# Performance work log

Hardware: AMD Instinct MI355X
Metric: run time of the kernel (lower is better)

## Reference

```python
import jax, jax.numpy as jnp
import numpy as np

N = 50000
E_RAND = 800000
IN_DIM = 256
HID = 64
HEADS = 4
OUT_DIM = 256
NEG_SLOPE = 0.01  # torch F.leaky_relu default


def _xavier(key, shape, fan_in, fan_out):
    gain = np.sqrt(2.0)  # calculate_gain('relu')
    std = gain * np.sqrt(2.0 / (fan_in + fan_out))
    return jax.random.normal(key, shape, dtype=jnp.float32) * std


def setup_inputs() -> dict:
    key = jax.random.key(0)
    k = jax.random.split(key, 8)
    h = jax.random.normal(k[0], (N, IN_DIM), dtype=jnp.float32)
    # random edges + self-loops so every node has in-degree >= 1
    src = jnp.concatenate([jax.random.randint(k[1], (E_RAND,), 0, N), jnp.arange(N)]).astype(jnp.int32)
    dst = jnp.concatenate([jax.random.randint(k[2], (E_RAND,), 0, N), jnp.arange(N)]).astype(jnp.int32)
    # layer1: HEADS independent GAT heads, hidden HID each
    W1 = _xavier(k[3], (HEADS, HID, IN_DIM), IN_DIM, HID)          # fc.weight per head
    a1 = _xavier(k[4], (HEADS, 2 * HID), 2 * HID, 1)               # attn_fc.weight per head
    # layer2: single head, in = HID*HEADS, out = OUT_DIM
    W2 = _xavier(k[5], (OUT_DIM, HID * HEADS), HID * HEADS, OUT_DIM)
    a2 = _xavier(k[6], (2 * OUT_DIM,), 2 * OUT_DIM, 1)
    return {"h": h, "W1": W1, "a1": a1, "W2": W2, "a2": a2, "src": src, "dst": dst}


def _leaky(x):
    return jnp.where(x > 0, x, NEG_SLOPE * x)


def _segment_softmax(e, dst, n):
    # e: [E, ...] logits per edge; softmax over edges sharing the same dst node
    m = jax.ops.segment_max(e, dst, num_segments=n)
    m = jnp.where(jnp.isfinite(m), m, 0.0)  # guard empty segments
    ex = jnp.exp(e - m[dst])
    s = jax.ops.segment_sum(ex, dst, num_segments=n)
    return ex / s[dst]


def reference(h, W1, a1, W2, a2, src, dst):
    n = h.shape[0]
    # ---- layer1: multi-head GAT, merge='cat' ----
    z = jnp.einsum('ni,hoi->nho', h, W1)                 # [N,H,HID]
    a_s, a_d = a1[:, :HID], a1[:, HID:]                  # split cat([src,dst]) linear
    es = jnp.einsum('nho,ho->nh', z, a_s)                # per-node src score
    ed = jnp.einsum('nho,ho->nh', z, a_d)                # per-node dst score
    e = _leaky(es[src] + ed[dst])                        # [E,H]
    alpha = _segment_softmax(e, dst, n)                  # segment softmax per dst
    m = jax.ops.segment_sum(alpha[:, :, None] * z[src], dst, num_segments=n)  # [N,H,HID]
    h1 = jax.nn.elu(m.reshape(n, HEADS * HID))
    # ---- layer2: single-head GAT ----
    z2 = h1 @ W2.T                                       # [N,OUT]
    e2 = _leaky((z2 @ a2[:OUT_DIM])[src] + (z2 @ a2[OUT_DIM:])[dst])  # [E]
    alpha2 = _segment_softmax(e2, dst, n)
    out = jax.ops.segment_sum(alpha2[:, None] * z2[src], dst, num_segments=n)  # [N,OUT]
    return out
```

## Files before the change

kernel.cpp:

```cpp
#include <hip/hip_runtime.h>
#include <hip/hip_bf16.h>
#include <math.h>

#define NEG 0.01f
#define MAXDEG 128

typedef __attribute__((ext_vector_type(4))) unsigned u32x4;
typedef __attribute__((ext_vector_type(4))) float f32x4;

__device__ __forceinline__ float wmax_all(float v){
#pragma unroll
  for (int o=32;o>0;o>>=1) v = fmaxf(v, __shfl_xor(v,o,64));
  return v;
}
__device__ __forceinline__ float wsum_all(float v){
#pragma unroll
  for (int o=32;o>0;o>>=1) v += __shfl_xor(v,o,64);
  return v;
}
__device__ __forceinline__ int wred_sum_i(int v){
#pragma unroll
  for (int o=32;o>0;o>>=1) v += __shfl_down(v,o,64);
  return v;
}
__device__ __forceinline__ float bf_lo(unsigned u){ union{unsigned i;float f;} c; c.i=u<<16; return c.f; }
__device__ __forceinline__ float bf_hi(unsigned u){ union{unsigned i;float f;} c; c.i=u&0xffff0000u; return c.f; }
__device__ __forceinline__ unsigned short f2bf(float f){
  union{float f; unsigned i;} c; c.f=f;
  unsigned r = c.i + 0x7fffu + ((c.i>>16)&1u);
  return (unsigned short)(r>>16);
}
__device__ __forceinline__ float leaky1(float x){ return x>0.f? x : NEG*x; }

__device__ __forceinline__ void mfma16(f32x4& d, u32x4 a, u32x4 b){
  asm volatile("v_mfma_f32_16x16x32_bf16 %0, %1, %2, %0" : "+v"(d) : "v"(a), "v"(b));
}

__global__ void zero_cnt_k(int* __restrict__ cnt, int n){
  int i = blockIdx.x*blockDim.x + threadIdx.x;
  if (i<n) cnt[i]=0;
}

__global__ void hist_k(const int* __restrict__ dst, int* __restrict__ cnt, int E){
  int i = blockIdx.x*blockDim.x+threadIdx.x;
  if (i<E) atomicAdd(&cnt[dst[i]], 1);
}

__global__ void scan_partial_k(const int* __restrict__ cnt, int* __restrict__ bsum, int n){
  int b = blockIdx.x, t = threadIdx.x;
  int base = b*1024 + t*4;
  int s=0;
#pragma unroll
  for (int i=0;i<4;i++){ int idx=base+i; if(idx<n) s+=cnt[idx]; }
  int ws = wred_sum_i(s);
  __shared__ int sw[4];
  int wave=t>>6, lane=t&63;
  if (lane==0) sw[wave]=ws;
  __syncthreads();
  if (t==0) bsum[b] = sw[0]+sw[1]+sw[2]+sw[3];
}

__global__ void scan_bsums_k(const int* __restrict__ bsum, int* __restrict__ bpre,
                             int nb, int* __restrict__ row_off, int n, int E){
  if (threadIdx.x==0 && blockIdx.x==0){
    int c=0;
    for (int i=0;i<nb;i++){ bpre[i]=c; c+=bsum[i]; }
    row_off[n]=E;
  }
}

__global__ void scan_final_k(const int* __restrict__ cnt, const int* __restrict__ bpre,
                             int* __restrict__ row_off, int* __restrict__ cursor, int n){
  int b=blockIdx.x, t=threadIdx.x;
  int lane=t&63, wave=t>>6;
  int base=b*1024 + t*4;
  int v[4]; int ts=0;
#pragma unroll
  for (int i=0;i<4;i++){ int idx=base+i; v[i]=(idx<n)?cnt[idx]:0; ts+=v[i]; }
  int x=ts;
#pragma unroll
  for (int o=1;o<64;o<<=1){ int y=__shfl_up(x,o,64); if (lane>=o) x+=y; }
  __shared__ int sw[4];
  if (lane==63) sw[wave]=x;
  __syncthreads();
  int wpre=0;
  for (int w=0;w<wave;w++) wpre+=sw[w];
  int run = bpre[b] + wpre + (x - ts);
#pragma unroll
  for (int i=0;i<4;i++){ int idx=base+i; if(idx<n){ row_off[idx]=run; cursor[idx]=run; } run+=v[i]; }
}

__global__ void scatter_k(const int* __restrict__ src, const int* __restrict__ dst,
                          int* __restrict__ cursor, int* __restrict__ col, int E){
  int i=blockIdx.x*blockDim.x+threadIdx.x;
  if (i<E){ int slot=atomicAdd(&cursor[dst[i]],1); col[slot]=src[i]; }
}

__global__ void conv_h_k(const float* __restrict__ h, unsigned short* __restrict__ Ab,
                         int n_elems, int npad_elems){
  int i = blockIdx.x*blockDim.x + threadIdx.x;
  int base = i*8;
  if (base >= npad_elems) return;
  unsigned short u[8];
  if (base + 8 <= n_elems){
    float4 x = *(const float4*)(h+base);
    float4 y = *(const float4*)(h+base+4);
    u[0]=f2bf(x.x);u[1]=f2bf(x.y);u[2]=f2bf(x.z);u[3]=f2bf(x.w);
    u[4]=f2bf(y.x);u[5]=f2bf(y.y);u[6]=f2bf(y.z);u[7]=f2bf(y.w);
  } else {
#pragma unroll
    for (int j=0;j<8;j++) u[j]=0;
  }
  uint4 o;
  o.x=(unsigned)u[0]|((unsigned)u[1]<<16); o.y=(unsigned)u[2]|((unsigned)u[3]<<16);
  o.z=(unsigned)u[4]|((unsigned)u[5]<<16); o.w=(unsigned)u[6]|((unsigned)u[7]<<16);
  *(uint4*)(Ab+base)=o;
}

__global__ void conv_w_k(const float* __restrict__ W1, const float* __restrict__ W2,
                         unsigned short* __restrict__ Wb){
  int i = blockIdx.x*blockDim.x + threadIdx.x;
  int base = i*8;
  const float* src = (base<65536)? (W1+base) : (W2+(base-65536));
  float4 x=*(const float4*)src, y=*(const float4*)(src+4);
  unsigned short u[8];
  u[0]=f2bf(x.x);u[1]=f2bf(x.y);u[2]=f2bf(x.z);u[3]=f2bf(x.w);
  u[4]=f2bf(y.x);u[5]=f2bf(y.y);u[6]=f2bf(y.z);u[7]=f2bf(y.w);
  uint4 o;
  o.x=(unsigned)u[0]|((unsigned)u[1]<<16); o.y=(unsigned)u[2]|((unsigned)u[3]<<16);
  o.z=(unsigned)u[4]|((unsigned)u[5]<<16); o.w=(unsigned)u[6]|((unsigned)u[7]<<16);
  *(uint4*)(Wb+base)=o;
}

template<int L>
__global__ __launch_bounds__(256) void gemm_mfma(const unsigned short* __restrict__ Ab,
    const unsigned short* __restrict__ Wb, const float* __restrict__ av,
    unsigned short* __restrict__ zb, float* __restrict__ eS, float* __restrict__ eD){
  __shared__ char lds[40960];
  const int tid=threadIdx.x, lane=tid&63, w=tid>>6;
  const int r15=lane&15, kg=lane>>4;
  const int bm = blockIdx.x*64;
  const char* Ag = (const char*)Ab + (size_t)bm*512;
  const char* Bg = (const char*)Wb;
  auto stage=[&](int kt){
#pragma unroll
    for (int i=0;i<2;i++){
      int o=tid*16+i*4096, row=o>>7, cb=o&127;
      uint4 v = *(const uint4*)(Ag + (size_t)row*512 + kt*128 + cb);
      *(uint4*)(lds + (o ^ ((row&7)<<4))) = v;
    }
#pragma unroll
    for (int i=0;i<8;i++){
      int o=tid*16+i*4096, row=o>>7, cb=o&127;
      uint4 v = *(const uint4*)(Bg + (size_t)row*512 + kt*128 + cb);
      *(uint4*)(lds + 8192 + (o ^ ((row&7)<<4))) = v;
    }
  };
  f32x4 acc[4][4];
  f32x4 z4 = {0.f,0.f,0.f,0.f};
#pragma unroll
  for (int m=0;m<4;m++)
#pragma unroll
    for (int n=0;n<4;n++) acc[m][n]=z4;

  for (int kt=0;kt<4;kt++){
    if (kt) __syncthreads();
    stage(kt);
    __syncthreads();
#pragma unroll
    for (int kk=0;kk<2;kk++){
      u32x4 af[4], bf[4];
#pragma unroll
      for (int m=0;m<4;m++){
        int row = m*16 + r15;
        int off = row*128 + kk*64 + kg*16;
        af[m] = *(const u32x4*)(lds + (off ^ ((row&7)<<4)));
      }
#pragma unroll
      for (int n=0;n<4;n++){
        int c = w*64 + n*16 + r15;
        int off = c*128 + kk*64 + kg*16;
        bf[n] = *(const u32x4*)(lds + 8192 + (off ^ ((c&7)<<4)));
      }
#pragma unroll
      for (int m=0;m<4;m++)
#pragma unroll
        for (int n=0;n<4;n++) mfma16(acc[m][n], af[m], bf[n]);
    }
  }
  asm volatile("s_nop 7\n\ts_nop 7");
  float avs[4], avd[4];
#pragma unroll
  for (int n=0;n<4;n++){
    int c = n*16 + r15;
    if (L==1){ avs[n]=av[w*128 + c];      avd[n]=av[w*128 + 64 + c]; }
    else     { avs[n]=av[w*64 + c];       avd[n]=av[256 + w*64 + c]; }
  }
  __syncthreads();
  float* s_ep = (float*)lds;
#pragma unroll
  for (int m=0;m<4;m++)
#pragma unroll
    for (int j=0;j<4;j++){
      float pe=0.f, pd=0.f;
#pragma unroll
      for (int n=0;n<4;n++){ pe += acc[m][n][j]*avs[n]; pd += acc[m][n][j]*avd[n]; }
#pragma unroll
      for (int o=1;o<16;o<<=1){ pe += __shfl_xor(pe,o,64); pd += __shfl_xor(pd,o,64); }
      if (r15==0){
        int lrow = m*16 + kg*4 + j;
        if (L==1){ eS[(size_t)(bm+lrow)*4 + w]=pe; eD[(size_t)(bm+lrow)*4 + w]=pd; }
        else     { s_ep[(w*64+lrow)*2]=pe; s_ep[(w*64+lrow)*2+1]=pd; }
      }
    }
  if (L==2){
    __syncthreads();
    if (tid<64){
      float se = s_ep[(0*64+tid)*2]+s_ep[(1*64+tid)*2]+s_ep[(2*64+tid)*2]+s_ep[(3*64+tid)*2];
      float sd = s_ep[(0*64+tid)*2+1]+s_ep[(1*64+tid)*2+1]+s_ep[(2*64+tid)*2+1]+s_ep[(3*64+tid)*2+1];
      eS[bm+tid]=se; eD[bm+tid]=sd;
    }
  }
#pragma unroll
  for (int m=0;m<4;m++)
#pragma unroll
    for (int n=0;n<4;n++)
#pragma unroll
      for (int j=0;j<4;j++){
        float v0 = acc[m][n][j];
        float v1 = __shfl_down(v0,1,64);
        if (!(lane&1)){
          unsigned pk = (unsigned)f2bf(v0) | ((unsigned)f2bf(v1)<<16);
          int row = bm + m*16 + kg*4 + j, cc = w*64 + n*16 + r15;
          *(unsigned*)(zb + (size_t)row*256 + cc) = pk;
        }
      }
}

__global__ __launch_bounds__(256) void agg1_k(const unsigned short* __restrict__ zb,
    const float* __restrict__ es, const float* __restrict__ ed,
    const int* __restrict__ row_off, const int* __restrict__ col,
    unsigned short* __restrict__ h1b, int n){
  __shared__ int   s_src[4][MAXDEG];
  __shared__ float s_al [4][MAXDEG][4];
  int w = threadIdx.x>>6, lane = threadIdx.x&63;
  int nd = blockIdx.x*4 + w;
  if (nd>=n) return;
  int beg=row_off[nd], deg=row_off[nd+1]-beg;
  float4 edv = *(const float4*)(ed + (size_t)nd*4);
  float m0=-1e30f,m1=-1e30f,m2=-1e30f,m3=-1e30f;
  for (int j=lane;j<deg;j+=64){
    int s=col[beg+j];
    float4 ev = *((const float4*)es + s);
    ev.x=leaky1(ev.x+edv.x); ev.y=leaky1(ev.y+edv.y);
    ev.z=leaky1(ev.z+edv.z); ev.w=leaky1(ev.w+edv.w);
    if (j<MAXDEG){
      s_src[w][j]=s;
      s_al[w][j][0]=ev.x; s_al[w][j][1]=ev.y; s_al[w][j][2]=ev.z; s_al[w][j][3]=ev.w;
    }
    m0=fmaxf(m0,ev.x); m1=fmaxf(m1,ev.y); m2=fmaxf(m2,ev.z); m3=fmaxf(m3,ev.w);
  }
  m0=wmax_all(m0); m1=wmax_all(m1); m2=wmax_all(m2); m3=wmax_all(m3);
  float t0=0.f,t1=0.f,t2=0.f,t3=0.f;
  for (int j=lane;j<deg;j+=64){
    float e0,e1,e2,e3;
    if (j<MAXDEG){ e0=s_al[w][j][0]; e1=s_al[w][j][1]; e2=s_al[w][j][2]; e3=s_al[w][j][3]; }
    else {
      int s=col[beg+j];
      float4 ev = *((const float4*)es + s);
      e0=leaky1(ev.x+edv.x); e1=leaky1(ev.y+edv.y); e2=leaky1(ev.z+edv.z); e3=leaky1(ev.w+edv.w);
    }
    e0=__expf(e0-m0); e1=__expf(e1-m1); e2=__expf(e2-m2); e3=__expf(e3-m3);
    if (j<MAXDEG){ s_al[w][j][0]=e0; s_al[w][j][1]=e1; s_al[w][j][2]=e2; s_al[w][j][3]=e3; }
    t0+=e0; t1+=e1; t2+=e2; t3+=e3;
  }
  t0=wsum_all(t0); t1=wsum_all(t1); t2=wsum_all(t2); t3=wsum_all(t3);
  int hh = lane>>4;
  float invh = 1.0f/(hh==0? t0 : hh==1? t1 : hh==2? t2 : t3);
  float mh   = (hh==0? m0 : hh==1? m1 : hh==2? m2 : m3);
  const uint2* zp = (const uint2*)zb;
  float a0=0.f,a1a=0.f,a2a=0.f,a3=0.f;
  int dm = deg<MAXDEG? deg:MAXDEG;
  int j=0;
  for (; j+2<=dm; j+=2){
    int sA=s_src[w][j], sB=s_src[w][j+1];
    float alA=s_al[w][j][hh], alB=s_al[w][j+1][hh];
    uint2 vA = zp[(size_t)((unsigned)sA*64u + (unsigned)lane)];
    uint2 vB = zp[(size_t)((unsigned)sB*64u + (unsigned)lane)];
    a0 += alA*bf_lo(vA.x); a1a += alA*bf_hi(vA.x);
    a2a += alA*bf_lo(vA.y); a3 += alA*bf_hi(vA.y);
    a0 += alB*bf_lo(vB.x); a1a += alB*bf_hi(vB.x);
    a2a += alB*bf_lo(vB.y); a3 += alB*bf_hi(vB.y);
  }
  for (; j<dm; j++){
    int s=s_src[w][j];
    float al=s_al[w][j][hh];
    uint2 v = zp[(size_t)((unsigned)s*64u + (unsigned)lane)];
    a0 += al*bf_lo(v.x); a1a += al*bf_hi(v.x);
    a2a += al*bf_lo(v.y); a3 += al*bf_hi(v.y);
  }
  for (; j<deg; j++){
    int s=col[beg+j];
    float4 ev = *((const float4*)es + s);
    float e = (hh==0? ev.x+edv.x : hh==1? ev.y+edv.y : hh==2? ev.z+edv.z : ev.w+edv.w);
    float al = __expf(leaky1(e)-mh);
    uint2 v = zp[(size_t)((unsigned)s*64u + (unsigned)lane)];
    a0 += al*bf_lo(v.x); a1a += al*bf_hi(v.x);
    a2a += al*bf_lo(v.y); a3 += al*bf_hi(v.y);
  }
  a0*=invh; a1a*=invh; a2a*=invh; a3*=invh;
  a0 = a0>0.f? a0 : __expf(a0)-1.0f;
  a1a= a1a>0.f? a1a: __expf(a1a)-1.0f;
  a2a= a2a>0.f? a2a: __expf(a2a)-1.0f;
  a3 = a3>0.f? a3 : __expf(a3)-1.0f;
  unsigned lo = (unsigned)f2bf(a0) | ((unsigned)f2bf(a1a)<<16);
  unsigned hi = (unsigned)f2bf(a2a) | ((unsigned)f2bf(a3)<<16);
  *(uint2*)(h1b + (size_t)nd*256 + lane*4) = make_uint2(lo,hi);
}

__global__ __launch_bounds__(256) void agg2_k(const unsigned short* __restrict__ zb,
    const float* __restrict__ e2s, const float* __restrict__ e2d,
    const int* __restrict__ row_off, const int* __restrict__ col,
    float* __restrict__ out, int n){
  __shared__ int   s_src[4][MAXDEG];
  __shared__ float s_al [4][MAXDEG];
  int w = threadIdx.x>>6, lane = threadIdx.x&63;
  int nd = blockIdx.x*4 + w;
  if (nd>=n) return;
  int beg=row_off[nd], deg=row_off[nd+1]-beg;
  float edv = e2d[nd];
  float m=-1e30f;
  for (int j=lane;j<deg;j+=64){
    int s=col[beg+j];
    float ev = leaky1(e2s[s]+edv);
    if (j<MAXDEG){ s_src[w][j]=s; s_al[w][j]=ev; }
    m=fmaxf(m,ev);
  }
  m=wmax_all(m);
  float ts=0.f;
  for (int j=lane;j<deg;j+=64){
    float e;
    if (j<MAXDEG) e=s_al[w][j];
    else { int s=col[beg+j]; e=leaky1(e2s[s]+edv); }
    e=__expf(e-m);
    if (j<MAXDEG) s_al[w][j]=e;
    ts+=e;
  }
  ts=wsum_all(ts);
  float inv=1.0f/ts;
  const uint2* zp = (const uint2*)zb;
  float a0=0.f,a1a=0.f,a2a=0.f,a3=0.f;
  int dm = deg<MAXDEG? deg:MAXDEG;
  int j=0;
  for (; j+2<=dm; j+=2){
    int sA=s_src[w][j], sB=s_src[w][j+1];
    float alA=s_al[w][j], alB=s_al[w][j+1];
    uint2 vA = zp[(size_t)((unsigned)sA*64u + (unsigned)lane)];
    uint2 vB = zp[(size_t)((unsigned)sB*64u + (unsigned)lane)];
    a0 += alA*bf_lo(vA.x); a1a += alA*bf_hi(vA.x);
    a2a += alA*bf_lo(vA.y); a3 += alA*bf_hi(vA.y);
    a0 += alB*bf_lo(vB.x); a1a += alB*bf_hi(vB.x);
    a2a += alB*bf_lo(vB.y); a3 += alB*bf_hi(vB.y);
  }
  for (; j<dm; j++){
    int s=s_src[w][j];
    float al=s_al[w][j];
    uint2 v = zp[(size_t)((unsigned)s*64u + (unsigned)lane)];
    a0 += al*bf_lo(v.x); a1a += al*bf_hi(v.x);
    a2a += al*bf_lo(v.y); a3 += al*bf_hi(v.y);
  }
  for (; j<deg; j++){
    int s=col[beg+j];
    float al = __expf(leaky1(e2s[s]+edv)-m);
    uint2 v = zp[(size_t)((unsigned)s*64u + (unsigned)lane)];
    a0 += al*bf_lo(v.x); a1a += al*bf_hi(v.x);
    a2a += al*bf_lo(v.y); a3 += al*bf_hi(v.y);
  }
  *((float4*)out + (size_t)nd*64 + lane) = make_float4(a0*inv,a1a*inv,a2a*inv,a3*inv);
}

extern "C" void kernel_launch(void* const* d_in, const int* in_sizes, int n_in,
                              void* d_out, int out_size, void* d_ws, size_t ws_size,
                              hipStream_t stream){
  const float* h  = (const float*)d_in[0];
  const float* W1 = (const float*)d_in[1];
  const float* a1 = (const float*)d_in[2];
  const float* W2 = (const float*)d_in[3];
  const float* a2 = (const float*)d_in[4];
  const int* src  = (const int*)d_in[5];
  const int* dst  = (const int*)d_in[6];
  float* out = (float*)d_out;
  int N = in_sizes[0]/256;
  int E = in_sizes[5];
  int Npad = ((N+63)/64)*64;

  char* p=(char*)d_ws;
  auto alloc=[&](size_t bytes)->void*{ void* r=(void*)p; p += (bytes+255)&~(size_t)255; return r; };
  unsigned short* Ab  =(unsigned short*)alloc(sizeof(unsigned short)*(size_t)Npad*256);
  unsigned short* zb  =(unsigned short*)alloc(sizeof(unsigned short)*(size_t)Npad*256);
  unsigned short* z2b =(unsigned short*)alloc(sizeof(unsigned short)*(size_t)Npad*256);
  unsigned short* h1b =(unsigned short*)alloc(sizeof(unsigned short)*(size_t)Npad*256);
  unsigned short* Wb  =(unsigned short*)alloc(sizeof(unsigned short)*131072);
  float* es  =(float*)alloc(sizeof(float)*(size_t)Npad*4);
  float* ed  =(float*)alloc(sizeof(float)*(size_t)Npad*4);
  float* e2s =(float*)alloc(sizeof(float)*(size_t)Npad);
  float* e2d =(float*)alloc(sizeof(float)*(size_t)Npad);
  int* cnt    =(int*)alloc(sizeof(int)*(size_t)N);
  int* row_off=(int*)alloc(sizeof(int)*(size_t)(N+1));
  int* cursor =(int*)alloc(sizeof(int)*(size_t)N);
  int* col    =(int*)alloc(sizeof(int)*(size_t)E);
  int* bsum   =(int*)alloc(sizeof(int)*64);
  int* bpre   =(int*)alloc(sizeof(int)*64);

  int nb = (N+1023)/1024;

  zero_cnt_k<<<(N+255)/256,256,0,stream>>>(cnt,N);
  hist_k<<<(E+255)/256,256,0,stream>>>(dst,cnt,E);
  scan_partial_k<<<nb,256,0,stream>>>(cnt,bsum,N);
  scan_bsums_k<<<1,64,0,stream>>>(bsum,bpre,nb,row_off,N,E);
  scan_final_k<<<nb,256,0,stream>>>(cnt,bpre,row_off,cursor,N);
  scatter_k<<<(E+255)/256,256,0,stream>>>(src,dst,cursor,col,E);

  conv_h_k<<<(Npad*32+255)/256,256,0,stream>>>(h,Ab,N*256,Npad*256);
  conv_w_k<<<64,256,0,stream>>>(W1,W2,Wb);

  int gblocks = Npad/64;
  gemm_mfma<1><<<gblocks,256,0,stream>>>(Ab, Wb, a1, zb, es, ed);
  agg1_k<<<(N+3)/4,256,0,stream>>>(zb,es,ed,row_off,col,h1b,N);
  gemm_mfma<2><<<gblocks,256,0,stream>>>(h1b, Wb+65536, a2, z2b, e2s, e2d);
  agg2_k<<<(N+3)/4,256,0,stream>>>(z2b,e2s,e2d,row_off,col,out,N);
}
```

Before: 299.0 us.

## Fuse fp32-to-bf16 input conversion into GEMM staging, use hardware bf16 pack, unroll gathers

Drops the separate conv_h kernel and bf16 buffer for h. The layer-1 GEMM now loads fp32 rows straight from h and converts them with v_cvt_pk_bf16_f32 while staging tiles into LDS, clamping out-of-range rows to the last valid row. The software round-to-nearest bf16 packing is replaced by the hardware pack instruction in every kernel, and the aggregation gather loops are unrolled from 2 to 4 neighbours to keep more loads in flight. In exchange the GEMM reads twice the bytes for A and does the conversion inside its critical path.

```diff
diff --git a/kernel.cpp b/kernel.cpp
--- a/kernel.cpp
+++ b/kernel.cpp
@@ -29,6 +29,11 @@
   union{float f; unsigned i;} c; c.f=f;
   unsigned r = c.i + 0x7fffu + ((c.i>>16)&1u);
   return (unsigned short)(r>>16);
+}
+__device__ __forceinline__ unsigned cvtpk(float lo, float hi){
+  unsigned r;
+  asm("v_cvt_pk_bf16_f32 %0, %1, %2" : "=v"(r) : "v"(lo), "v"(hi));
+  return r;
 }
 __device__ __forceinline__ float leaky1(float x){ return x>0.f? x : NEG*x; }
 
@@ -96,57 +101,43 @@
   if (i<E){ int slot=atomicAdd(&cursor[dst[i]],1); col[slot]=src[i]; }
 }
 
-__global__ void conv_h_k(const float* __restrict__ h, unsigned short* __restrict__ Ab,
-                         int n_elems, int npad_elems){
-  int i = blockIdx.x*blockDim.x + threadIdx.x;
-  int base = i*8;
-  if (base >= npad_elems) return;
-  unsigned short u[8];
-  if (base + 8 <= n_elems){
-    float4 x = *(const float4*)(h+base);
-    float4 y = *(const float4*)(h+base+4);
-    u[0]=f2bf(x.x);u[1]=f2bf(x.y);u[2]=f2bf(x.z);u[3]=f2bf(x.w);
-    u[4]=f2bf(y.x);u[5]=f2bf(y.y);u[6]=f2bf(y.z);u[7]=f2bf(y.w);
-  } else {
-#pragma unroll
-    for (int j=0;j<8;j++) u[j]=0;
-  }
-  uint4 o;
-  o.x=(unsigned)u[0]|((unsigned)u[1]<<16); o.y=(unsigned)u[2]|((unsigned)u[3]<<16);
-  o.z=(unsigned)u[4]|((unsigned)u[5]<<16); o.w=(unsigned)u[6]|((unsigned)u[7]<<16);
-  *(uint4*)(Ab+base)=o;
-}
-
 __global__ void conv_w_k(const float* __restrict__ W1, const float* __restrict__ W2,
                          unsigned short* __restrict__ Wb){
   int i = blockIdx.x*blockDim.x + threadIdx.x;
   int base = i*8;
   const float* src = (base<65536)? (W1+base) : (W2+(base-65536));
   float4 x=*(const float4*)src, y=*(const float4*)(src+4);
-  unsigned short u[8];
-  u[0]=f2bf(x.x);u[1]=f2bf(x.y);u[2]=f2bf(x.z);u[3]=f2bf(x.w);
-  u[4]=f2bf(y.x);u[5]=f2bf(y.y);u[6]=f2bf(y.z);u[7]=f2bf(y.w);
   uint4 o;
-  o.x=(unsigned)u[0]|((unsigned)u[1]<<16); o.y=(unsigned)u[2]|((unsigned)u[3]<<16);
-  o.z=(unsigned)u[4]|((unsigned)u[5]<<16); o.w=(unsigned)u[6]|((unsigned)u[7]<<16);
+  o.x=cvtpk(x.x,x.y); o.y=cvtpk(x.z,x.w);
+  o.z=cvtpk(y.x,y.y); o.w=cvtpk(y.z,y.w);
   *(uint4*)(Wb+base)=o;
 }
 
 template<int L>
-__global__ __launch_bounds__(256) void gemm_mfma(const unsigned short* __restrict__ Ab,
+__global__ __launch_bounds__(256) void gemm_mfma(const void* __restrict__ Aptr,
     const unsigned short* __restrict__ Wb, const float* __restrict__ av,
-    unsigned short* __restrict__ zb, float* __restrict__ eS, float* __restrict__ eD){
+    unsigned short* __restrict__ zb, float* __restrict__ eS, float* __restrict__ eD, int n){
   __shared__ char lds[40960];
   const int tid=threadIdx.x, lane=tid&63, w=tid>>6;
   const int r15=lane&15, kg=lane>>4;
   const int bm = blockIdx.x*64;
-  const char* Ag = (const char*)Ab + (size_t)bm*512;
-  const char* Bg = (const char*)Wb;
+  const float* Af = (const float*)Aptr;
+  const char*  Ag = (const char*)Aptr + (size_t)bm*512;
+  const char*  Bg = (const char*)Wb;
   auto stage=[&](int kt){
 #pragma unroll
     for (int i=0;i<2;i++){
       int o=tid*16+i*4096, row=o>>7, cb=o&127;
-      uint4 v = *(const uint4*)(Ag + (size_t)row*512 + kt*128 + cb);
+      uint4 v;
+      if (L==1){
+        int gr = bm+row; if (gr>=n) gr=n-1;
+        const float* s = Af + (size_t)gr*256 + kt*64 + (cb>>1);
+        float4 x=*(const float4*)s, y=*(const float4*)(s+4);
+        v.x=cvtpk(x.x,x.y); v.y=cvtpk(x.z,x.w);
+        v.z=cvtpk(y.x,y.y); v.w=cvtpk(y.z,y.w);
+      } else {
+        v = *(const uint4*)(Ag + (size_t)row*512 + kt*128 + cb);
+      }
       *(uint4*)(lds + (o ^ ((row&7)<<4))) = v;
     }
 #pragma unroll
@@ -161,7 +152,7 @@
 #pragma unroll
   for (int m=0;m<4;m++)
 #pragma unroll
-    for (int n=0;n<4;n++) acc[m][n]=z4;
+    for (int n2=0;n2<4;n2++) acc[m][n2]=z4;
 
   for (int kt=0;kt<4;kt++){
     if (kt) __syncthreads();
@@ -177,24 +168,24 @@
         af[m] = *(const u32x4*)(lds + (off ^ ((row&7)<<4)));
       }
 #pragma unroll
-      for (int n=0;n<4;n++){
-        int c = w*64 + n*16 + r15;
+      for (int n2=0;n2<4;n2++){
+        int c = w*64 + n2*16 + r15;
         int off = c*128 + kk*64 + kg*16;
-        bf[n] = *(const u32x4*)(lds + 8192 + (off ^ ((c&7)<<4)));
+        bf[n2] = *(const u32x4*)(lds + 8192 + (off ^ ((c&7)<<4)));
       }
 #pragma unroll
       for (int m=0;m<4;m++)
 #pragma unroll
-        for (int n=0;n<4;n++) mfma16(acc[m][n], af[m], bf[n]);
+        for (int n2=0;n2<4;n2++) mfma16(acc[m][n2], af[m], bf[n2]);
     }
   }
   asm volatile("s_nop 7\n\ts_nop 7");
   float avs[4], avd[4];
 #pragma unroll
-  for (int n=0;n<4;n++){
-    int c = n*16 + r15;
-    if (L==1){ avs[n]=av[w*128 + c];      avd[n]=av[w*128 + 64 + c]; }
-    else     { avs[n]=av[w*64 + c];       avd[n]=av[256 + w*64 + c]; }
+  for (int n2=0;n2<4;n2++){
+    int c = n2*16 + r15;
+    if (L==1){ avs[n2]=av[w*128 + c];      avd[n2]=av[w*128 + 64 + c]; }
+    else     { avs[n2]=av[w*64 + c];       avd[n2]=av[256 + w*64 + c]; }
   }
   __syncthreads();
   float* s_ep = (float*)lds;
@@ -204,7 +195,7 @@
     for (int j=0;j<4;j++){
       float pe=0.f, pd=0.f;
 #pragma unroll
-      for (int n=0;n<4;n++){ pe += acc[m][n][j]*avs[n]; pd += acc[m][n][j]*avd[n]; }
+      for (int n2=0;n2<4;n2++){ pe += acc[m][n2][j]*avs[n2]; pd += acc[m][n2][j]*avd[n2]; }
 #pragma unroll
       for (int o=1;o<16;o<<=1){ pe += __shfl_xor(pe,o,64); pd += __shfl_xor(pd,o,64); }
       if (r15==0){
@@ -224,14 +215,14 @@
 #pragma unroll
   for (int m=0;m<4;m++)
 #pragma unroll
-    for (int n=0;n<4;n++)
+    for (int n2=0;n2<4;n2++)
 #pragma unroll
       for (int j=0;j<4;j++){
-        float v0 = acc[m][n][j];
+        float v0 = acc[m][n2][j];
         float v1 = __shfl_down(v0,1,64);
         if (!(lane&1)){
-          unsigned pk = (unsigned)f2bf(v0) | ((unsigned)f2bf(v1)<<16);
-          int row = bm + m*16 + kg*4 + j, cc = w*64 + n*16 + r15;
+          unsigned pk = cvtpk(v0,v1);
+          int row = bm + m*16 + kg*4 + j, cc = w*64 + n2*16 + r15;
           *(unsigned*)(zb + (size_t)row*256 + cc) = pk;
         }
       }
@@ -282,15 +273,18 @@
   float a0=0.f,a1a=0.f,a2a=0.f,a3=0.f;
   int dm = deg<MAXDEG? deg:MAXDEG;
   int j=0;
-  for (; j+2<=dm; j+=2){
-    int sA=s_src[w][j], sB=s_src[w][j+1];
-    float alA=s_al[w][j][hh], alB=s_al[w][j+1][hh];
-    uint2 vA = zp[(size_t)((unsigned)sA*64u + (unsigned)lane)];
-    uint2 vB = zp[(size_t)((unsigned)sB*64u + (unsigned)lane)];
-    a0 += alA*bf_lo(vA.x); a1a += alA*bf_hi(vA.x);
-    a2a += alA*bf_lo(vA.y); a3 += alA*bf_hi(vA.y);
-    a0 += alB*bf_lo(vB.x); a1a += alB*bf_hi(vB.x);
-    a2a += alB*bf_lo(vB.y); a3 += alB*bf_hi(vB.y);
+  for (; j+4<=dm; j+=4){
+    int s0=s_src[w][j],   s1=s_src[w][j+1], s2=s_src[w][j+2], s3=s_src[w][j+3];
+    float b0=s_al[w][j][hh],   b1=s_al[w][j+1][hh];
+    float b2=s_al[w][j+2][hh], b3=s_al[w][j+3][hh];
+    uint2 v0 = zp[(size_t)((unsigned)s0*64u + (unsigned)lane)];
+    uint2 v1 = zp[(size_t)((unsigned)s1*64u + (unsigned)lane)];
+    uint2 v2 = zp[(size_t)((unsigned)s2*64u + (unsigned)lane)];
+    uint2 v3 = zp[(size_t)((unsigned)s3*64u + (unsigned)lane)];
+    a0 += b0*bf_lo(v0.x); a1a += b0*bf_hi(v0.x); a2a += b0*bf_lo(v0.y); a3 += b0*bf_hi(v0.y);
+    a0 += b1*bf_lo(v1.x); a1a += b1*bf_hi(v1.x); a2a += b1*bf_lo(v1.y); a3 += b1*bf_hi(v1.y);
+    a0 += b2*bf_lo(v2.x); a1a += b2*bf_hi(v2.x); a2a += b2*bf_lo(v2.y); a3 += b2*bf_hi(v2.y);
+    a0 += b3*bf_lo(v3.x); a1a += b3*bf_hi(v3.x); a2a += b3*bf_lo(v3.y); a3 += b3*bf_hi(v3.y);
   }
   for (; j<dm; j++){
     int s=s_src[w][j];
@@ -313,9 +307,7 @@
   a1a= a1a>0.f? a1a: __expf(a1a)-1.0f;
   a2a= a2a>0.f? a2a: __expf(a2a)-1.0f;
   a3 = a3>0.f? a3 : __expf(a3)-1.0f;
-  unsigned lo = (unsigned)f2bf(a0) | ((unsigned)f2bf(a1a)<<16);
-  unsigned hi = (unsigned)f2bf(a2a) | ((unsigned)f2bf(a3)<<16);
-  *(uint2*)(h1b + (size_t)nd*256 + lane*4) = make_uint2(lo,hi);
+  *(uint2*)(h1b + (size_t)nd*256 + lane*4) = make_uint2(cvtpk(a0,a1a), cvtpk(a2a,a3));
 }
 
 __global__ __launch_bounds__(256) void agg2_k(const unsigned short* __restrict__ zb,
@@ -352,15 +344,17 @@
   float a0=0.f,a1a=0.f,a2a=0.f,a3=0.f;
   int dm = deg<MAXDEG? deg:MAXDEG;
   int j=0;
-  for (; j+2<=dm; j+=2){
-    int sA=s_src[w][j], sB=s_src[w][j+1];
-    float alA=s_al[w][j], alB=s_al[w][j+1];
-    uint2 vA = zp[(size_t)((unsigned)sA*64u + (unsigned)lane)];
-    uint2 vB = zp[(size_t)((unsigned)sB*64u + (unsigned)lane)];
-    a0 += alA*bf_lo(vA.x); a1a += alA*bf_hi(vA.x);
-    a2a += alA*bf_lo(vA.y); a3 += alA*bf_hi(vA.y);
-    a0 += alB*bf_lo(vB.x); a1a += alB*bf_hi(vB.x);
-    a2a += alB*bf_lo(vB.y); a3 += alB*bf_hi(vB.y);
+  for (; j+4<=dm; j+=4){
+    int s0=s_src[w][j],   s1=s_src[w][j+1], s2=s_src[w][j+2], s3=s_src[w][j+3];
+    float b0=s_al[w][j],   b1=s_al[w][j+1], b2=s_al[w][j+2], b3=s_al[w][j+3];
+    uint2 v0 = zp[(size_t)((unsigned)s0*64u + (unsigned)lane)];
+    uint2 v1 = zp[(size_t)((unsigned)s1*64u + (unsigned)lane)];
+    uint2 v2 = zp[(size_t)((unsigned)s2*64u + (unsigned)lane)];
+    uint2 v3 = zp[(size_t)((unsigned)s3*64u + (unsigned)lane)];
+    a0 += b0*bf_lo(v0.x); a1a += b0*bf_hi(v0.x); a2a += b0*bf_lo(v0.y); a3 += b0*bf_hi(v0.y);
+    a0 += b1*bf_lo(v1.x); a1a += b1*bf_hi(v1.x); a2a += b1*bf_lo(v1.y); a3 += b1*bf_hi(v1.y);
+    a0 += b2*bf_lo(v2.x); a1a += b2*bf_hi(v2.x); a2a += b2*bf_lo(v2.y); a3 += b2*bf_hi(v2.y);
+    a0 += b3*bf_lo(v3.x); a1a += b3*bf_hi(v3.x); a2a += b3*bf_lo(v3.y); a3 += b3*bf_hi(v3.y);
   }
   for (; j<dm; j++){
     int s=s_src[w][j];
@@ -396,7 +390,6 @@
 
   char* p=(char*)d_ws;
   auto alloc=[&](size_t bytes)->void*{ void* r=(void*)p; p += (bytes+255)&~(size_t)255; return r; };
-  unsigned short* Ab  =(unsigned short*)alloc(sizeof(unsigned short)*(size_t)Npad*256);
   unsigned short* zb  =(unsigned short*)alloc(sizeof(unsigned short)*(size_t)Npad*256);
   unsigned short* z2b =(unsigned short*)alloc(sizeof(unsigned short)*(size_t)Npad*256);
   unsigned short* h1b =(unsigned short*)alloc(sizeof(unsigned short)*(size_t)Npad*256);
@@ -421,12 +414,11 @@
   scan_final_k<<<nb,256,0,stream>>>(cnt,bpre,row_off,cursor,N);
   scatter_k<<<(E+255)/256,256,0,stream>>>(src,dst,cursor,col,E);
 
-  conv_h_k<<<(Npad*32+255)/256,256,0,stream>>>(h,Ab,N*256,Npad*256);
   conv_w_k<<<64,256,0,stream>>>(W1,W2,Wb);
 
   int gblocks = Npad/64;
-  gemm_mfma<1><<<gblocks,256,0,stream>>>(Ab, Wb, a1, zb, es, ed);
+  gemm_mfma<1><<<gblocks,256,0,stream>>>((const void*)h,   Wb,       a1, zb,  es,  ed,  N);
   agg1_k<<<(N+3)/4,256,0,stream>>>(zb,es,ed,row_off,col,h1b,N);
-  gemm_mfma<2><<<gblocks,256,0,stream>>>(h1b, Wb+65536, a2, z2b, e2s, e2d);
+  gemm_mfma<2><<<gblocks,256,0,stream>>>((const void*)h1b, Wb+65536, a2, z2b, e2s, e2d, N);
   agg2_k<<<(N+3)/4,256,0,stream>>>(z2b,e2s,e2d,row_off,col,out,N);
 }
```

Result: faster. 287.1 us (-4.0%).
